# Optimization experiments

Measured on AMD Instinct MI355X. Metric: run time of the kernel, lower is better.

Reference implementation:

```python
import jax, jax.numpy as jnp
import numpy as np

D_MODEL = 1024
NUM_HEADS = 16
HEAD_DIM = D_MODEL // NUM_HEADS

def _trunc_normal(key, shape, std):
    # truncated normal in [-3*std, 3*std]
    return jax.random.truncated_normal(key, -3.0, 3.0, shape, dtype=jnp.float32) * std

def setup_inputs() -> dict:
    key = jax.random.key(0)
    kx, kq, kk, kv, ko = jax.random.split(key, 5)
    std = np.sqrt(2.0 / (D_MODEL + D_MODEL))
    return {
        "in_features": jax.random.normal(kx, (4, 2048, D_MODEL), dtype=jnp.float32),
        "weight_q": _trunc_normal(kq, (D_MODEL, D_MODEL), std),
        "weight_k": _trunc_normal(kk, (D_MODEL, D_MODEL), std),
        "weight_v": _trunc_normal(kv, (D_MODEL, D_MODEL), std),
        "weight_o": _trunc_normal(ko, (D_MODEL, D_MODEL), std),
    }

def reference(in_features, weight_q, weight_k, weight_v, weight_o):
    in_dtype = in_features.dtype
    x = in_features.astype(jnp.float32)
    B, S, _ = x.shape
    # projections: x @ W.T (matches torch matmul(x, weight.T))
    Q = x @ weight_q.T
    K = x @ weight_k.T
    V = x @ weight_v.T
    # [B, H, S, hd]
    Q = Q.reshape(B, S, NUM_HEADS, HEAD_DIM).transpose(0, 2, 1, 3)
    K = K.reshape(B, S, NUM_HEADS, HEAD_DIM).transpose(0, 2, 1, 3)
    V = V.reshape(B, S, NUM_HEADS, HEAD_DIM).transpose(0, 2, 1, 3)
    scores = jnp.einsum('bhqd,bhkd->bhqk', Q, K) / jnp.sqrt(jnp.float32(HEAD_DIM))
    causal = jnp.tril(jnp.ones((S, S), dtype=bool))  # [S, S]
    scores = jnp.where(causal, scores, -jnp.inf)
    attn = jax.nn.softmax(scores, axis=-1)
    out = jnp.einsum('bhqk,bhkd->bhqd', attn, V)  # [B, H, S, hd]
    out = out.transpose(0, 2, 1, 3).reshape(B, S, D_MODEL)
    out = out @ weight_o.T
    return out.astype(in_dtype)
```

## Files before the change

### kernel.cpp

```cpp
#include <hip/hip_runtime.h>
#include <stdint.h>
#include <math.h>

#define B_SZ 4
#define S_LEN 2048
#define NH 16
#define HD 64
#define DM 1024
#define M_ROWS (B_SZ * S_LEN)
#define NQ 16

typedef __bf16 bf16x8 __attribute__((ext_vector_type(8)));
typedef __bf16 bf16x4 __attribute__((ext_vector_type(4)));
typedef float f32x4 __attribute__((ext_vector_type(4)));
typedef unsigned int u32x2 __attribute__((ext_vector_type(2)));

typedef __attribute__((address_space(3))) void lds_t;
typedef __attribute__((address_space(1))) const void gbl_t;

__device__ __forceinline__ unsigned cvtpk_bf16(float a, float b) {
  unsigned r;
  asm("v_cvt_pk_bf16_f32 %0, %1, %2" : "=v"(r) : "v"(a), "v"(b));
  return r;
}

__global__ void cvt_all(const float* __restrict__ x,
                        const float* __restrict__ wq, const float* __restrict__ wk,
                        const float* __restrict__ wv, const float* __restrict__ wo,
                        __bf16* __restrict__ xb, __bf16* __restrict__ wdst) {
  const int NX4 = M_ROWS * DM / 4;
  const int NW4 = DM * DM / 4;
  const int TOT = NX4 + 4 * NW4;
  int i = blockIdx.x * blockDim.x + threadIdx.x;
  int stride = gridDim.x * blockDim.x;
  for (; i < TOT; i += stride) {
    const float* src;
    __bf16* dst;
    int idx;
    if (i < NX4) {
      src = x; dst = xb; idx = i;
    } else {
      int j = i - NX4;
      int sel = j >> 18;
      src = (sel == 0) ? wq : (sel == 1) ? wk : (sel == 2) ? wv : wo;
      dst = wdst + (size_t)sel * DM * DM;
      idx = j & (NW4 - 1);
    }
    f32x4 v = reinterpret_cast<const f32x4*>(src)[idx];
    bf16x4 o;
    o[0] = (__bf16)v[0]; o[1] = (__bf16)v[1];
    o[2] = (__bf16)v[2]; o[3] = (__bf16)v[3];
    reinterpret_cast<bf16x4*>(dst)[idx] = o;
  }
}

template <int MODE>
__global__ __launch_bounds__(256, 2) void gemm64(
    const unsigned short* __restrict__ A, const unsigned short* __restrict__ BT,
    __bf16* __restrict__ Qb, __bf16* __restrict__ Kb, __bf16* __restrict__ Vt,
    float* __restrict__ Out, int NX) {
  __shared__ __align__(16) unsigned short As[2][128 * 64];
  __shared__ __align__(16) unsigned short Bs[2][128 * 64];

  const int t = threadIdx.x, lane = t & 63, w = t >> 6;
  const int wm = w >> 1, wn = w & 1;
  const int g = lane >> 4, c = lane & 15;

  const int nwg = (int)gridDim.x;
  const int cpx = nwg >> 3;
  const int bid = (int)blockIdx.x;
  const int wg = (bid & 7) * cpx + (bid >> 3);
  const int bx = wg % NX, by = wg / NX;
  const int tm0 = by * 128, tn0 = bx * 128;
  const int K = DM;

  const int srow = t >> 3;
  const int scolb = (t & 7) << 4;
  const int ssw = scolb ^ ((srow & 7) << 4);
  const uint8_t* gA0 = (const uint8_t*)A + ((size_t)(tm0 + srow) * K) * 2 + ssw;
  const uint8_t* gB0 = (const uint8_t*)BT + ((size_t)(tn0 + srow) * K) * 2 + ssw;
  const int kxor = (c & 7) << 4;

#define STAGE(buf_, k0_) do {                                                  \
    uint8_t* lA = (uint8_t*)&As[buf_][0] + t * 16;                             \
    uint8_t* lB = (uint8_t*)&Bs[buf_][0] + t * 16;                             \
    _Pragma("unroll") for (int q = 0; q < 4; ++q) {                            \
      __builtin_amdgcn_global_load_lds(                                        \
          (gbl_t*)(gA0 + ((size_t)q * 32 * K + (k0_)) * 2),                    \
          (lds_t*)(lA + q * 4096), 16, 0, 0);                                  \
      __builtin_amdgcn_global_load_lds(                                        \
          (gbl_t*)(gB0 + ((size_t)q * 32 * K + (k0_)) * 2),                    \
          (lds_t*)(lB + q * 4096), 16, 0, 0);                                  \
    }                                                                          \
  } while (0)

  f32x4 acc[4][4] = {};

  STAGE(0, 0);
  __syncthreads();

  const int NT = K / 64;
  for (int kt = 0; kt < NT; ++kt) {
    const int cur = kt & 1;
    if (kt + 1 < NT) STAGE(cur ^ 1, (kt + 1) * 64);

#pragma unroll
    for (int ks = 0; ks < 2; ++ks) {
      bf16x8 af[4], bfm[4];
#pragma unroll
      for (int mb = 0; mb < 4; ++mb)
        af[mb] = *reinterpret_cast<const bf16x8*>(
            (const uint8_t*)&As[cur][0] + (wm * 64 + mb * 16 + c) * 128 + ((ks * 64 + g * 16) ^ kxor));
#pragma unroll
      for (int nb = 0; nb < 4; ++nb)
        bfm[nb] = *reinterpret_cast<const bf16x8*>(
            (const uint8_t*)&Bs[cur][0] + (wn * 64 + nb * 16 + c) * 128 + ((ks * 64 + g * 16) ^ kxor));
      __builtin_amdgcn_s_setprio(1);
#pragma unroll
      for (int mb = 0; mb < 4; ++mb)
#pragma unroll
        for (int nb = 0; nb < 4; ++nb)
          acc[mb][nb] = __builtin_amdgcn_mfma_f32_16x16x32_bf16(af[mb], bfm[nb], acc[mb][nb], 0, 0, 0);
      __builtin_amdgcn_s_setprio(0);
    }
    __syncthreads();
  }
#undef STAGE

  const int rm0 = tm0 + wm * 64;
  const int cn0 = tn0 + wn * 64;
  const int sel = tn0 >> 10;
#pragma unroll
  for (int mb = 0; mb < 4; ++mb) {
#pragma unroll
    for (int nb = 0; nb < 4; ++nb) {
      f32x4 v = acc[mb][nb];
#pragma unroll
      for (int j = 0; j < 4; ++j) {
        int rm = rm0 + mb * 16 + g * 4 + j;
        int cn = cn0 + nb * 16 + c;
        float val = v[j];
        if (MODE == 0) {
          int b = rm >> 11, s = rm & 2047;
          int dmn = cn & 1023;
          int h = dmn >> 6, d = dmn & 63;
          if (sel == 0) {
            Qb[(((size_t)(b * NH + h) * S_LEN + s) << 6) + d] = (__bf16)(val * 0.125f);
          } else if (sel == 1) {
            Kb[(((size_t)(b * NH + h) * S_LEN + s) << 6) + d] = (__bf16)val;
          } else {
            Vt[((size_t)(b * NH + h) * HD + d) * S_LEN + s] = (__bf16)val;
          }
        } else {
          Out[(size_t)rm * DM + cn] = val;
        }
      }
    }
  }
}

template <int SPLIT>
__global__ __launch_bounds__(256, 3) void attn_kernel(
    const unsigned short* __restrict__ Qb, const unsigned short* __restrict__ Kb,
    const unsigned short* __restrict__ Vt, __bf16* __restrict__ Aout,
    __bf16* __restrict__ AP, float* __restrict__ Lp) {
  __shared__ __align__(16) unsigned short KVs[2][8192];
  __shared__ __align__(16) unsigned short Ps[4][32 * 72];

  const int t = threadIdx.x, lane = t & 63, w = t >> 6;
  const int g = lane >> 4, c = lane & 15;
  const int bh = blockIdx.y;
  const int qx = (NQ - 1) - (int)blockIdx.x / SPLIT;
  const int sp = (int)blockIdx.x % SPLIT;
  const int b = bh >> 4, h = bh & 15;
  const int q0 = qx * 128 + w * 32;

  const unsigned short* Qp = Qb + (size_t)bh * S_LEN * HD;
  const uint8_t* Kg8 = (const uint8_t*)(Kb + (size_t)bh * S_LEN * HD);
  const uint8_t* Vg8 = (const uint8_t*)(Vt + (size_t)bh * HD * S_LEN);

  const int sr = t >> 3;
  const int scb = ((t & 7) << 4) ^ ((sr & 7) << 4);
  const uint8_t* Kst = Kg8 + (size_t)sr * 128 + scb;
  const uint8_t* Vst = Vg8 + (size_t)sr * (S_LEN * 2) + scb;
  uint8_t* Ls = (uint8_t*)&KVs[0][0];

#define STAGE(buf, kvb_) do {                                                  \
    uint8_t* kd = Ls + (buf) * 16384 + t * 16;                                 \
    const uint8_t* kg = Kst + (size_t)(kvb_) * 128;                            \
    const uint8_t* vg = Vst + (size_t)(kvb_) * 2;                              \
    __builtin_amdgcn_global_load_lds((gbl_t*)kg, (lds_t*)kd, 16, 0, 0);        \
    __builtin_amdgcn_global_load_lds((gbl_t*)(kg + 32 * 128),                  \
                                     (lds_t*)(kd + 4096), 16, 0, 0);           \
    __builtin_amdgcn_global_load_lds((gbl_t*)vg, (lds_t*)(kd + 8192), 16, 0, 0);\
    __builtin_amdgcn_global_load_lds((gbl_t*)(vg + (size_t)32 * S_LEN * 2),    \
                                     (lds_t*)(kd + 12288), 16, 0, 0);          \
  } while (0)

  bf16x8 qf[2][2];
#pragma unroll
  for (int mb = 0; mb < 2; ++mb)
#pragma unroll
    for (int ks = 0; ks < 2; ++ks)
      qf[mb][ks] = *reinterpret_cast<const bf16x8*>(
          Qp + (size_t)(q0 + mb * 16 + c) * HD + ks * 32 + g * 8);

  bf16x8 onesf;
#pragma unroll
  for (int i = 0; i < 8; ++i) onesf[i] = (__bf16)1.0f;

  f32x4 oacc[2][4] = {};
  f32x4 lacc[2] = {};

  const int kxor = (c & 7) << 4;
  const int n_total = 2 * qx + 2;
  const int chunk = (n_total + SPLIT - 1) / SPLIT;
  int t0 = sp * chunk; if (t0 > n_total) t0 = n_total;
  int t1 = t0 + chunk; if (t1 > n_total) t1 = n_total;
  const int nblk_w = (q0 >> 6) + 1;

  const int st0 = (t0 < n_total) ? t0 : (n_total - 1);
  STAGE(0, st0 * 64);
  __syncthreads();

  __bf16* psw = (__bf16*)&Ps[w][0];
  const int qr = q0 + c;

  for (int kb = t0; kb < t1; ++kb) {
    const int cur = (kb - t0) & 1;
    if (kb + 1 < t1) STAGE(cur ^ 1, (kb + 1) * 64);

    if (kb < nblk_w) {
      const int kvb = kb * 64;
      const uint8_t* KL = Ls + cur * 16384;
      const uint8_t* VL = KL + 8192;

      f32x4 sacc[2][4] = {};
      __builtin_amdgcn_s_setprio(1);
#pragma unroll
      for (int ks = 0; ks < 2; ++ks) {
#pragma unroll
        for (int nb = 0; nb < 4; ++nb) {
          bf16x8 kf = *reinterpret_cast<const bf16x8*>(
              KL + (nb * 16 + c) * 128 + ((ks * 64 + g * 16) ^ kxor));
          sacc[0][nb] = __builtin_amdgcn_mfma_f32_16x16x32_bf16(kf, qf[0][ks], sacc[0][nb], 0, 0, 0);
          sacc[1][nb] = __builtin_amdgcn_mfma_f32_16x16x32_bf16(kf, qf[1][ks], sacc[1][nb], 0, 0, 0);
        }
      }
      __builtin_amdgcn_s_setprio(0);

      if (kb == nblk_w - 1) {
#pragma unroll
        for (int mb = 0; mb < 2; ++mb) {
          const int qrm = qr + mb * 16;
#pragma unroll
          for (int nb = 0; nb < 4; ++nb) {
            const int key0 = kvb + nb * 16 + g * 4;
            float p0 = (key0 + 0 <= qrm) ? __expf(sacc[mb][nb][0]) : 0.f;
            float p1 = (key0 + 1 <= qrm) ? __expf(sacc[mb][nb][1]) : 0.f;
            float p2 = (key0 + 2 <= qrm) ? __expf(sacc[mb][nb][2]) : 0.f;
            float p3 = (key0 + 3 <= qrm) ? __expf(sacc[mb][nb][3]) : 0.f;
            u32x2 pk = {cvtpk_bf16(p0, p1), cvtpk_bf16(p2, p3)};
            *reinterpret_cast<u32x2*>(psw + (mb * 16 + c) * 72 + nb * 16 + g * 4) = pk;
          }
        }
      } else {
#pragma unroll
        for (int mb = 0; mb < 2; ++mb)
#pragma unroll
          for (int nb = 0; nb < 4; ++nb) {
            float p0 = __expf(sacc[mb][nb][0]);
            float p1 = __expf(sacc[mb][nb][1]);
            float p2 = __expf(sacc[mb][nb][2]);
            float p3 = __expf(sacc[mb][nb][3]);
            u32x2 pk = {cvtpk_bf16(p0, p1), cvtpk_bf16(p2, p3)};
            *reinterpret_cast<u32x2*>(psw + (mb * 16 + c) * 72 + nb * 16 + g * 4) = pk;
          }
      }

      bf16x8 pf0_0 = *reinterpret_cast<const bf16x8*>(psw + (c) * 72 + g * 8);
      bf16x8 pf0_1 = *reinterpret_cast<const bf16x8*>(psw + (c) * 72 + 32 + g * 8);
      bf16x8 pf1_0 = *reinterpret_cast<const bf16x8*>(psw + (16 + c) * 72 + g * 8);
      bf16x8 pf1_1 = *reinterpret_cast<const bf16x8*>(psw + (16 + c) * 72 + 32 + g * 8);

      __builtin_amdgcn_s_setprio(1);
      lacc[0] = __builtin_amdgcn_mfma_f32_16x16x32_bf16(pf0_0, onesf, lacc[0], 0, 0, 0);
      lacc[0] = __builtin_amdgcn_mfma_f32_16x16x32_bf16(pf0_1, onesf, lacc[0], 0, 0, 0);
      lacc[1] = __builtin_amdgcn_mfma_f32_16x16x32_bf16(pf1_0, onesf, lacc[1], 0, 0, 0);
      lacc[1] = __builtin_amdgcn_mfma_f32_16x16x32_bf16(pf1_1, onesf, lacc[1], 0, 0, 0);

#pragma unroll
      for (int db = 0; db < 4; ++db) {
        bf16x8 vf0 = *reinterpret_cast<const bf16x8*>(
            VL + (db * 16 + c) * 128 + ((g * 16) ^ kxor));
        bf16x8 vf1 = *reinterpret_cast<const bf16x8*>(
            VL + (db * 16 + c) * 128 + ((64 + g * 16) ^ kxor));
        oacc[0][db] = __builtin_amdgcn_mfma_f32_16x16x32_bf16(pf0_0, vf0, oacc[0][db], 0, 0, 0);
        oacc[0][db] = __builtin_amdgcn_mfma_f32_16x16x32_bf16(pf0_1, vf1, oacc[0][db], 0, 0, 0);
        oacc[1][db] = __builtin_amdgcn_mfma_f32_16x16x32_bf16(pf1_0, vf0, oacc[1][db], 0, 0, 0);
        oacc[1][db] = __builtin_amdgcn_mfma_f32_16x16x32_bf16(pf1_1, vf1, oacc[1][db], 0, 0, 0);
      }
      __builtin_amdgcn_s_setprio(0);
    }
    __syncthreads();
  }
#undef STAGE

  if (SPLIT == 1) {
    float rl[2][4];
#pragma unroll
    for (int mb = 0; mb < 2; ++mb)
#pragma unroll
      for (int j = 0; j < 4; ++j) rl[mb][j] = 1.0f / lacc[mb][j];
#pragma unroll
    for (int mb = 0; mb < 2; ++mb)
#pragma unroll
      for (int db = 0; db < 4; ++db)
#pragma unroll
        for (int j = 0; j < 4; ++j) {
          float o = oacc[mb][db][j] * rl[mb][j];
          int s = q0 + mb * 16 + g * 4 + j;
          int d = db * 16 + c;
          Aout[(size_t)(b * S_LEN + s) * DM + h * HD + d] = (__bf16)o;
        }
  } else {
    __bf16* APs = AP + (size_t)(sp * (B_SZ * NH) + bh) * S_LEN * HD;
    float* Lps = Lp + (size_t)(sp * (B_SZ * NH) + bh) * S_LEN;
#pragma unroll
    for (int mb = 0; mb < 2; ++mb) {
#pragma unroll
      for (int db = 0; db < 4; ++db)
#pragma unroll
        for (int j = 0; j < 4; ++j) {
          int q = q0 + mb * 16 + g * 4 + j;
          APs[(size_t)q * HD + db * 16 + c] = (__bf16)oacc[mb][db][j];
        }
      if (c == 0) {
#pragma unroll
        for (int j = 0; j < 4; ++j)
          Lps[q0 + mb * 16 + g * 4 + j] = lacc[mb][j];
      }
    }
  }
}

__global__ void attn_combine4(const __bf16* __restrict__ AP, const float* __restrict__ Lp,
                              __bf16* __restrict__ Aout) {
  const int NIT = B_SZ * NH * S_LEN * (HD / 8);
  int i = blockIdx.x * blockDim.x + threadIdx.x;
  int stride = gridDim.x * blockDim.x;
  const size_t SOFF = (size_t)(B_SZ * NH) * S_LEN * HD;
  const size_t LOFF = (size_t)(B_SZ * NH) * S_LEN;
  for (; i < NIT; i += stride) {
    int d8 = i & 7;
    int q = (i >> 3) & (S_LEN - 1);
    int bh = i >> 14;
    size_t base = ((size_t)bh * S_LEN + q) * HD + d8 * 8;
    size_t lbase = (size_t)bh * S_LEN + q;
    float l = Lp[lbase] + Lp[LOFF + lbase] + Lp[2 * LOFF + lbase] + Lp[3 * LOFF + lbase];
    float rl = 1.0f / l;
    bf16x8 a0 = *reinterpret_cast<const bf16x8*>(AP + base);
    bf16x8 a1 = *reinterpret_cast<const bf16x8*>(AP + SOFF + base);
    bf16x8 a2 = *reinterpret_cast<const bf16x8*>(AP + 2 * SOFF + base);
    bf16x8 a3 = *reinterpret_cast<const bf16x8*>(AP + 3 * SOFF + base);
    int b = bh >> 4, h = bh & 15;
    bf16x8 o;
#pragma unroll
    for (int k = 0; k < 8; ++k)
      o[k] = (__bf16)((((float)a0[k] + (float)a1[k]) + ((float)a2[k] + (float)a3[k])) * rl);
    *reinterpret_cast<bf16x8*>(Aout + ((size_t)(b * S_LEN + q)) * DM + h * HD + d8 * 8) = o;
  }
}

extern "C" void kernel_launch(void* const* d_in, const int* in_sizes, int n_in,
                              void* d_out, int out_size, void* d_ws, size_t ws_size,
                              hipStream_t stream) {
  const float* x = (const float*)d_in[0];
  const float* wq = (const float*)d_in[1];
  const float* wk = (const float*)d_in[2];
  const float* wv = (const float*)d_in[3];
  const float* wo = (const float*)d_in[4];
  float* out = (float*)d_out;

  uint8_t* ws = (uint8_t*)d_ws;
  const size_t MB = 1024 * 1024;
  unsigned short* xb   = (unsigned short*)(ws);
  unsigned short* wcat = (unsigned short*)(ws + 16 * MB);
  unsigned short* wob  = (unsigned short*)(ws + 22 * MB);
  unsigned short* Qb   = (unsigned short*)(ws + 24 * MB);
  unsigned short* Kb   = (unsigned short*)(ws + 40 * MB);
  unsigned short* Vt   = (unsigned short*)(ws + 56 * MB);
  __bf16* AP           = (__bf16*)(ws + 72 * MB);
  float* Lp            = (float*)(ws + 16 * MB);

  cvt_all<<<2048, 256, 0, stream>>>(x, wq, wk, wv, wo, (__bf16*)xb, (__bf16*)wcat);

  gemm64<0><<<dim3((3 * DM / 128) * (M_ROWS / 128)), 256, 0, stream>>>(
      xb, wcat, (__bf16*)Qb, (__bf16*)Kb, (__bf16*)Vt, nullptr, 3 * DM / 128);

  __bf16* Aout = (__bf16*)xb;
  if (ws_size >= (size_t)136 * MB) {
    attn_kernel<4><<<dim3(NQ * 4, B_SZ * NH), 256, 0, stream>>>(
        Qb, Kb, Vt, Aout, AP, Lp);
    attn_combine4<<<2048, 256, 0, stream>>>(AP, Lp, Aout);
  } else {
    attn_kernel<1><<<dim3(NQ, B_SZ * NH), 256, 0, stream>>>(
        Qb, Kb, Vt, Aout, nullptr, nullptr);
  }

  gemm64<1><<<dim3((DM / 128) * (M_ROWS / 128)), 256, 0, stream>>>(
      xb, wob, nullptr, nullptr, nullptr, out, DM / 128);
}
```

Baseline: 203.0 us.

## Single-buffer GEMM LDS tiles to raise occupancy to three blocks per CU

Drops the double-buffered LDS staging in the projection GEMM and uses a single A/B tile, with a load-then-sync-then-compute loop. The launch bound rises from 2 to 3 blocks per CU. This halves LDS per block, so more workgroups can be resident and hide latency by interleaving across blocks. In exchange, the prefetch of the next K tile no longer overlaps with the MFMA work inside a block, and each iteration now needs two barriers.

```diff
diff --git a/kernel.cpp b/kernel.cpp
--- a/kernel.cpp
+++ b/kernel.cpp
@@ -55,12 +55,12 @@
 }
 
 template <int MODE>
-__global__ __launch_bounds__(256, 2) void gemm64(
+__global__ __launch_bounds__(256, 3) void gemm64(
     const unsigned short* __restrict__ A, const unsigned short* __restrict__ BT,
     __bf16* __restrict__ Qb, __bf16* __restrict__ Kb, __bf16* __restrict__ Vt,
     float* __restrict__ Out, int NX) {
-  __shared__ __align__(16) unsigned short As[2][128 * 64];
-  __shared__ __align__(16) unsigned short Bs[2][128 * 64];
+  __shared__ __align__(16) unsigned short As[128 * 64];
+  __shared__ __align__(16) unsigned short Bs[128 * 64];
 
   const int t = threadIdx.x, lane = t & 63, w = t >> 6;
   const int wm = w >> 1, wn = w & 1;
@@ -79,30 +79,21 @@
   const int ssw = scolb ^ ((srow & 7) << 4);
   const uint8_t* gA0 = (const uint8_t*)A + ((size_t)(tm0 + srow) * K) * 2 + ssw;
   const uint8_t* gB0 = (const uint8_t*)BT + ((size_t)(tn0 + srow) * K) * 2 + ssw;
+  uint8_t* lA0 = (uint8_t*)As + t * 16;
+  uint8_t* lB0 = (uint8_t*)Bs + t * 16;
   const int kxor = (c & 7) << 4;
 
-#define STAGE(buf_, k0_) do {                                                  \
-    uint8_t* lA = (uint8_t*)&As[buf_][0] + t * 16;                             \
-    uint8_t* lB = (uint8_t*)&Bs[buf_][0] + t * 16;                             \
-    _Pragma("unroll") for (int q = 0; q < 4; ++q) {                            \
-      __builtin_amdgcn_global_load_lds(                                        \
-          (gbl_t*)(gA0 + ((size_t)q * 32 * K + (k0_)) * 2),                    \
-          (lds_t*)(lA + q * 4096), 16, 0, 0);                                  \
-      __builtin_amdgcn_global_load_lds(                                        \
-          (gbl_t*)(gB0 + ((size_t)q * 32 * K + (k0_)) * 2),                    \
-          (lds_t*)(lB + q * 4096), 16, 0, 0);                                  \
-    }                                                                          \
-  } while (0)
-
   f32x4 acc[4][4] = {};
 
-  STAGE(0, 0);
-  __syncthreads();
-
-  const int NT = K / 64;
-  for (int kt = 0; kt < NT; ++kt) {
-    const int cur = kt & 1;
-    if (kt + 1 < NT) STAGE(cur ^ 1, (kt + 1) * 64);
+  for (int k0 = 0; k0 < K; k0 += 64) {
+#pragma unroll
+    for (int q = 0; q < 4; ++q) {
+      __builtin_amdgcn_global_load_lds((gbl_t*)(gA0 + ((size_t)q * 32 * K + k0) * 2),
+                                       (lds_t*)(lA0 + q * 4096), 16, 0, 0);
+      __builtin_amdgcn_global_load_lds((gbl_t*)(gB0 + ((size_t)q * 32 * K + k0) * 2),
+                                       (lds_t*)(lB0 + q * 4096), 16, 0, 0);
+    }
+    __syncthreads();
 
 #pragma unroll
     for (int ks = 0; ks < 2; ++ks) {
@@ -110,11 +101,11 @@
 #pragma unroll
       for (int mb = 0; mb < 4; ++mb)
         af[mb] = *reinterpret_cast<const bf16x8*>(
-            (const uint8_t*)&As[cur][0] + (wm * 64 + mb * 16 + c) * 128 + ((ks * 64 + g * 16) ^ kxor));
+            (const uint8_t*)As + (wm * 64 + mb * 16 + c) * 128 + ((ks * 64 + g * 16) ^ kxor));
 #pragma unroll
       for (int nb = 0; nb < 4; ++nb)
         bfm[nb] = *reinterpret_cast<const bf16x8*>(
-            (const uint8_t*)&Bs[cur][0] + (wn * 64 + nb * 16 + c) * 128 + ((ks * 64 + g * 16) ^ kxor));
+            (const uint8_t*)Bs + (wn * 64 + nb * 16 + c) * 128 + ((ks * 64 + g * 16) ^ kxor));
       __builtin_amdgcn_s_setprio(1);
 #pragma unroll
       for (int mb = 0; mb < 4; ++mb)
@@ -125,7 +116,6 @@
     }
     __syncthreads();
   }
-#undef STAGE
 
   const int rm0 = tm0 + wm * 64;
   const int cn0 = tn0 + wn * 64;
```

Result: no change. 204.6 us (+0.8%).
